# Performance work log

Measured on AMD Instinct MI355X. Metric: run time of the kernel, lower is better.

The kernel has to match this reference:

```python
import jax, jax.numpy as jnp
import numpy as np

B, T, D, H = 4, 2048, 1024, 16
DH = D // H

def setup_inputs() -> dict:
    key = jax.random.key(0)
    k1, k2, k3 = jax.random.split(key, 3)
    x = jax.random.normal(k1, (B, T, D), dtype=jnp.float32)
    w_qkv = jax.random.normal(k2, (D, 3 * D), dtype=jnp.float32) * (1.0 / np.sqrt(D))
    w_out = jax.random.normal(k3, (D, D), dtype=jnp.float32) * (1.0 / np.sqrt(D))
    return {"x": x, "w_qkv": w_qkv, "w_out": w_out}

def reference(x, w_qkv, w_out):
    Bq, Tq, C = x.shape
    qkv = x @ w_qkv                                   # [B,T,3D]
    q, k, v = jnp.split(qkv, 3, axis=-1)
    q = q.reshape(Bq, Tq, H, DH).transpose(0, 2, 1, 3)  # [B,H,T,dh]
    k = k.reshape(Bq, Tq, H, DH).transpose(0, 2, 1, 3)
    v = v.reshape(Bq, Tq, H, DH).transpose(0, 2, 1, 3)
    scores = jnp.einsum('bhqd,bhkd->bhqk', q, k) / jnp.sqrt(jnp.float32(DH))
    mask = jnp.tril(jnp.ones((Tq, Tq), dtype=bool))
    scores = jnp.where(mask, scores, jnp.float32(-jnp.inf))
    attn = jax.nn.softmax(scores, axis=-1)
    out = jnp.einsum('bhqk,bhkd->bhqd', attn, v)      # [B,H,T,dh]
    out = out.transpose(0, 2, 1, 3).reshape(Bq, Tq, C)
    return out @ w_out
```

## Files before the change

### kernel.cpp

```cpp
#include <hip/hip_runtime.h>

#define B_ 4
#define T_ 2048
#define D_ 1024
#define H_ 16
#define DH_ 64
#define BH_ (B_*H_)
#define M_ (B_*T_)
#define N3_ (3*D_)

typedef __attribute__((ext_vector_type(8))) __bf16 bf16x8;
typedef __attribute__((ext_vector_type(4))) float f32x4;
typedef __attribute__((ext_vector_type(16))) float f32x16;
typedef __attribute__((ext_vector_type(8))) unsigned short u16x8;
typedef __attribute__((ext_vector_type(4))) unsigned short u16x4;
typedef int i32x2 __attribute__((ext_vector_type(2)));

__device__ inline void gload_lds16(const void* g, void* l) {
  __builtin_amdgcn_global_load_lds((const __attribute__((address_space(1))) void*)g,
                                   (__attribute__((address_space(3))) void*)l, 16, 0, 0);
}

__device__ inline unsigned short f2bf(float v) {
  __bf16 t = (__bf16)v;
  return *(unsigned short*)&t;
}

__device__ inline unsigned pk2(float lo, float hi2) {
  return (unsigned)f2bf(lo) | ((unsigned)f2bf(hi2) << 16);
}

template<int BASE>
__device__ inline bf16x8 buildP(const f32x16& S) {
  unsigned a = pk2(S[BASE+0], S[BASE+1]);
  unsigned b = pk2(S[BASE+2], S[BASE+3]);
  unsigned c = pk2(S[BASE+4], S[BASE+5]);
  unsigned d = pk2(S[BASE+6], S[BASE+7]);
  i32x2 r0 = __builtin_amdgcn_permlane32_swap((int)a, (int)c, false, false);
  i32x2 r1 = __builtin_amdgcn_permlane32_swap((int)b, (int)d, false, false);
  union { unsigned u[4]; bf16x8 v; } U;
  U.u[0] = (unsigned)r0[0];
  U.u[1] = (unsigned)r1[0];
  U.u[2] = (unsigned)r0[1];
  U.u[3] = (unsigned)r1[1];
  return U.v;
}

__global__ void prep(const float* __restrict__ x, unsigned short* __restrict__ xb,
                     const float* __restrict__ wq, unsigned short* __restrict__ wqT,
                     const float* __restrict__ wo, unsigned short* __restrict__ woT) {
  __shared__ unsigned short lds[64][72];
  int bid = blockIdx.x, tid = threadIdx.x;
  if (bid < 4096) {
    int i = bid * 256 + tid;
    const float4* p = (const float4*)(x + (size_t)i * 8);
    float4 a = p[0], b = p[1];
    float v[8] = {a.x, a.y, a.z, a.w, b.x, b.y, b.z, b.w};
    u16x8 r;
#pragma unroll
    for (int j = 0; j < 8; ++j) r[j] = f2bf(v[j]);
    *(u16x8*)(xb + (size_t)i * 8) = r;
    return;
  }
  const float* w;
  unsigned short* wt;
  int n0, k0, Ndim;
  if (bid < 4096 + 768) {
    int b2 = bid - 4096;
    w = wq; wt = wqT; Ndim = N3_;
    n0 = (b2 % 48) * 64; k0 = (b2 / 48) * 64;
  } else {
    int b3 = bid - 4864;
    w = wo; wt = woT; Ndim = D_;
    n0 = (b3 % 16) * 64; k0 = (b3 / 16) * 64;
  }
#pragma unroll
  for (int i = 0; i < 2; ++i) {
    int idx = i * 256 + tid;
    int r = idx >> 3, c8 = idx & 7;
    const float4* src = (const float4*)(w + (size_t)(k0 + r) * Ndim + n0 + c8 * 8);
    float4 a = src[0], b = src[1];
    float v[8] = {a.x, a.y, a.z, a.w, b.x, b.y, b.z, b.w};
#pragma unroll
    for (int j = 0; j < 8; ++j) lds[r][c8 * 8 + j] = f2bf(v[j]);
  }
  __syncthreads();
#pragma unroll
  for (int i = 0; i < 2; ++i) {
    int idx = i * 256 + tid;
    int r = idx >> 3, c8 = idx & 7;
    u16x8 o;
#pragma unroll
    for (int j = 0; j < 8; ++j) o[j] = lds[c8 * 8 + j][r];
    *(u16x8*)(wt + (size_t)(n0 + r) * 1024 + k0 + c8 * 8) = o;
  }
}

__global__ __launch_bounds__(512) void gemm8p(
    const unsigned short* __restrict__ A,
    const unsigned short* __restrict__ BT,
    int epi,
    unsigned short* __restrict__ qb, unsigned short* __restrict__ kb, unsigned short* __restrict__ vtb,
    float* __restrict__ outf) {
  extern __shared__ __align__(16) char lds[];
  const int tid = threadIdx.x;
  const int wave = tid >> 6, lane = tid & 63, g = lane >> 4, c = lane & 15;
  const int wm = wave >> 2, wn = wave & 3;
  int flat = blockIdx.y * gridDim.x + blockIdx.x;
  int xcd = flat & 7, local = flat >> 3;
  int bx = xcd * 8 + (local & 7);
  int by = local >> 3;
  const int m0 = bx * 128, n0 = by * 256;

  f32x4 acc[4][4] = {};

  auto stage3 = [&](int slot, int jj, int half) {
    char* sb = lds + slot * 49152;
#pragma unroll
    for (int q = 0; q < 3; ++q) {
      int qq = half * 3 + q;
      if (qq < 2) {
        int idx = qq * 512 + tid;
        int r = idx >> 3, s = idx & 7;
        gload_lds16(A + (size_t)(m0 + r) * 1024 + jj * 64 + 8 * (s ^ (r & 7)),
                    sb + idx * 16);
      } else {
        int idx = (qq - 2) * 512 + tid;
        int r = idx >> 3, s = idx & 7;
        gload_lds16(BT + (size_t)(n0 + r) * 1024 + jj * 64 + 8 * (s ^ (r & 7)),
                    sb + 16384 + idx * 16);
      }
    }
  };

  stage3(0, 0, 0); stage3(0, 0, 1);
  stage3(1, 1, 0); stage3(1, 1, 1);

  int sj = 0;
  for (int j = 0; j < 16; ++j) {
    const int jj = (j + 2 < 16) ? j + 2 : 15;
    int st2 = sj + 2; if (st2 >= 3) st2 -= 3;
    const char* sA = lds + sj * 49152;
    const char* sB = sA + 16384;

    stage3(st2, jj, 0);
    asm volatile("s_waitcnt vmcnt(9)" ::: "memory");
    __builtin_amdgcn_s_barrier();
    asm volatile("" ::: "memory");

    {
      bf16x8 af[4], bf[4];
#pragma unroll
      for (int mt = 0; mt < 4; ++mt) {
        int r = wm * 64 + mt * 16 + c;
        af[mt] = *(const bf16x8*)(sA + r * 128 + 16 * (g ^ (r & 7)));
      }
#pragma unroll
      for (int nt = 0; nt < 4; ++nt) {
        int r = wn * 64 + nt * 16 + c;
        bf[nt] = *(const bf16x8*)(sB + r * 128 + 16 * (g ^ (r & 7)));
      }
      __builtin_amdgcn_s_setprio(1);
#pragma unroll
      for (int mt = 0; mt < 4; ++mt)
#pragma unroll
        for (int nt = 0; nt < 4; ++nt)
          acc[mt][nt] = __builtin_amdgcn_mfma_f32_16x16x32_bf16(af[mt], bf[nt], acc[mt][nt], 0, 0, 0);
      __builtin_amdgcn_s_setprio(0);
    }

    stage3(st2, jj, 1);

    {
      bf16x8 af[4], bf[4];
#pragma unroll
      for (int mt = 0; mt < 4; ++mt) {
        int r = wm * 64 + mt * 16 + c;
        af[mt] = *(const bf16x8*)(sA + r * 128 + 16 * ((4 + g) ^ (r & 7)));
      }
#pragma unroll
      for (int nt = 0; nt < 4; ++nt) {
        int r = wn * 64 + nt * 16 + c;
        bf[nt] = *(const bf16x8*)(sB + r * 128 + 16 * ((4 + g) ^ (r & 7)));
      }
      __builtin_amdgcn_s_setprio(1);
#pragma unroll
      for (int mt = 0; mt < 4; ++mt)
#pragma unroll
        for (int nt = 0; nt < 4; ++nt)
          acc[mt][nt] = __builtin_amdgcn_mfma_f32_16x16x32_bf16(af[mt], bf[nt], acc[mt][nt], 0, 0, 0);
      __builtin_amdgcn_s_setprio(0);
    }

    __builtin_amdgcn_s_barrier();
    asm volatile("" ::: "memory");
    sj = sj + 1; if (sj >= 3) sj -= 3;
  }

  if (epi == 0) {
    int which = n0 >> 10;
    int colbase = n0 - (which << 10);
    if (which == 2) {
#pragma unroll
      for (int mt = 0; mt < 4; ++mt)
#pragma unroll
        for (int nt = 0; nt < 4; ++nt) {
          int m = m0 + wm * 64 + mt * 16 + g * 4;
          int n = colbase + wn * 64 + nt * 16 + c;
          int b = m >> 11, t = m & 2047;
          int h = n >> 6, d = n & 63;
          u16x4 pk;
#pragma unroll
          for (int i = 0; i < 4; ++i) pk[i] = f2bf(acc[mt][nt][i]);
          *(u16x4*)(vtb + ((size_t)(b * H_ + h) * 64 + d) * T_ + t) = pk;
        }
    } else {
      unsigned short* dst = which == 0 ? qb : kb;
      float scale = which == 0 ? 0.18033688011112042f : 1.0f;
#pragma unroll
      for (int mt = 0; mt < 4; ++mt)
#pragma unroll
        for (int nt = 0; nt < 4; ++nt)
#pragma unroll
          for (int i = 0; i < 4; ++i) {
            int m = m0 + wm * 64 + mt * 16 + g * 4 + i;
            int n = colbase + wn * 64 + nt * 16 + c;
            int b = m >> 11, t = m & 2047;
            int h = n >> 6, d = n & 63;
            dst[(((size_t)(b * H_ + h) * T_ + t) << 6) + d] = f2bf(acc[mt][nt][i] * scale);
          }
    }
  } else {
#pragma unroll
    for (int mt = 0; mt < 4; ++mt)
#pragma unroll
      for (int nt = 0; nt < 4; ++nt)
#pragma unroll
        for (int i = 0; i < 4; ++i) {
          int m = m0 + wm * 64 + mt * 16 + g * 4 + i;
          int n = n0 + wn * 64 + nt * 16 + c;
          outf[(size_t)m * 1024 + n] = acc[mt][nt][i];
        }
  }
}

#define PV_STEP(PF, KC)                                                                \
  {                                                                                    \
    bf16x8 pf = (PF);                                                                  \
    int dr0 = q32, dr1 = 32 + q32;                                                     \
    bf16x8 v0 = *(const bf16x8*)(sV + dr0 * 128 + 16 * (((KC)*2 + hi) ^ (dr0 & 7)));   \
    bf16x8 v1 = *(const bf16x8*)(sV + dr1 * 128 + 16 * (((KC)*2 + hi) ^ (dr1 & 7)));   \
    oT0 = __builtin_amdgcn_mfma_f32_32x32x16_bf16(v0, pf, oT0, 0, 0, 0);               \
    oT1 = __builtin_amdgcn_mfma_f32_32x32x16_bf16(v1, pf, oT1, 0, 0, 0);               \
  }

__global__ __launch_bounds__(512) void attn(
    const unsigned short* __restrict__ qbp,
    const unsigned short* __restrict__ kb,
    const unsigned short* __restrict__ vt,
    unsigned short* __restrict__ ao) {
  __shared__ __align__(16) char pool[49152];
  const int tid = threadIdx.x;
  const int wave = tid >> 6, lane = tid & 63;
  const int q32 = lane & 31, hi = lane >> 5;
  const int bh = blockIdx.y;
  const int flip = (bh >> 5) & 1;
  const int pb = flip ? blockIdx.x : (T_ / 256 - 1) - blockIdx.x;
  const int q0w = pb * 256 + wave * 32;
  const int kmax = 4 * pb + 3;
  const int dtile = 4 * pb + (wave >> 1);

  bf16x8 qf[4];
#pragma unroll
  for (int dhc = 0; dhc < 4; ++dhc)
    qf[dhc] = *(const bf16x8*)(qbp + ((size_t)bh * T_ + q0w + q32) * 64 + dhc * 16 + hi * 8);

  f32x16 oT0 = {}, oT1 = {};
  float l_run = 0.0f;

  auto stage = [&](int buf, int kt) {
    int r = tid >> 3, s8 = tid & 7;
    gload_lds16(kb + ((size_t)bh * T_ + kt * 64 + r) * 64 + 8 * (s8 ^ (r & 7)),
                pool + buf * 16384 + tid * 16);
    gload_lds16(vt + ((size_t)bh * 64 + r) * T_ + kt * 64 + 8 * (s8 ^ (r & 7)),
                pool + buf * 16384 + 8192 + tid * 16);
  };

  stage(0, 0);
  stage(1, 1);
  int sj = 0;
  for (int kt = 0; kt <= kmax; ++kt) {
    asm volatile("s_waitcnt vmcnt(2)" ::: "memory");
    __builtin_amdgcn_s_barrier();
    asm volatile("" ::: "memory");
    int st2 = sj + 2; if (st2 >= 3) st2 -= 3;
    if (kt + 2 <= kmax) stage(st2, kt + 2);
    if (kt <= dtile) {
      const char* sK = pool + sj * 16384;
      const char* sV = sK + 8192;

      f32x16 st0 = {}, st1 = {};
      __builtin_amdgcn_s_setprio(1);
#pragma unroll
      for (int dhc = 0; dhc < 4; ++dhc) {
        int kr0 = q32, kr1 = 32 + q32;
        bf16x8 k0 = *(const bf16x8*)(sK + kr0 * 128 + 16 * ((dhc * 2 + hi) ^ (kr0 & 7)));
        bf16x8 k1 = *(const bf16x8*)(sK + kr1 * 128 + 16 * ((dhc * 2 + hi) ^ (kr1 & 7)));
        st0 = __builtin_amdgcn_mfma_f32_32x32x16_bf16(k0, qf[dhc], st0, 0, 0, 0);
        st1 = __builtin_amdgcn_mfma_f32_32x32x16_bf16(k1, qf[dhc], st1, 0, 0, 0);
      }
      __builtin_amdgcn_s_setprio(0);

      if (kt == dtile) {
        int qg = q0w + q32;
#pragma unroll
        for (int r = 0; r < 16; ++r) {
          int krow = kt * 64 + (r & 3) + 8 * (r >> 2) + 4 * hi;
          if (krow > qg) st0[r] = -INFINITY;
          if (krow + 32 > qg) st1[r] = -INFINITY;
        }
      }

      float ps0 = 0.0f, ps1 = 0.0f, ps2 = 0.0f, ps3 = 0.0f;
#pragma unroll
      for (int r = 0; r < 16; r += 4) {
        float a0 = __builtin_amdgcn_exp2f(st0[r + 0]); st0[r + 0] = a0; ps0 += a0;
        float a1 = __builtin_amdgcn_exp2f(st0[r + 1]); st0[r + 1] = a1; ps1 += a1;
        float a2 = __builtin_amdgcn_exp2f(st0[r + 2]); st0[r + 2] = a2; ps2 += a2;
        float a3 = __builtin_amdgcn_exp2f(st0[r + 3]); st0[r + 3] = a3; ps3 += a3;
      }
#pragma unroll
      for (int r = 0; r < 16; r += 4) {
        float a0 = __builtin_amdgcn_exp2f(st1[r + 0]); st1[r + 0] = a0; ps0 += a0;
        float a1 = __builtin_amdgcn_exp2f(st1[r + 1]); st1[r + 1] = a1; ps1 += a1;
        float a2 = __builtin_amdgcn_exp2f(st1[r + 2]); st1[r + 2] = a2; ps2 += a2;
        float a3 = __builtin_amdgcn_exp2f(st1[r + 3]); st1[r + 3] = a3; ps3 += a3;
      }
      float ps = (ps0 + ps1) + (ps2 + ps3);
      ps += __shfl_xor(ps, 32);
      l_run += ps;

      __builtin_amdgcn_s_setprio(1);
      PV_STEP(buildP<0>(st0), 0)
      PV_STEP(buildP<8>(st0), 1)
      PV_STEP(buildP<0>(st1), 2)
      PV_STEP(buildP<8>(st1), 3)
      __builtin_amdgcn_s_setprio(0);
    }
    sj = sj + 1; if (sj >= 3) sj -= 3;
  }

  __syncthreads();
  unsigned short* ep = (unsigned short*)pool + wave * (32 * 72);
  float inv_l = 1.0f / l_run;
#pragma unroll
  for (int r = 0; r < 16; ++r) {
    int d0 = (r & 3) + 8 * (r >> 2) + 4 * hi;
    ep[q32 * 72 + d0]      = f2bf(oT0[r] * inv_l);
    ep[q32 * 72 + 32 + d0] = f2bf(oT1[r] * inv_l);
  }
  __syncthreads();
  {
    int q = lane >> 1, half = lane & 1;
    int t = q0w + q;
    int b = bh >> 4, h = bh & 15;
    const unsigned short* row = ep + q * 72 + half * 32;
    unsigned short* g = ao + ((size_t)(b * T_ + t)) * 1024 + h * 64 + half * 32;
#pragma unroll
    for (int j = 0; j < 4; ++j)
      *(u16x8*)(g + j * 8) = *(const u16x8*)(row + j * 8);
  }
}

extern "C" void kernel_launch(void* const* d_in, const int* in_sizes, int n_in,
                              void* d_out, int out_size, void* d_ws, size_t ws_size,
                              hipStream_t stream) {
  const float* x = (const float*)d_in[0];
  const float* w_qkv = (const float*)d_in[1];
  const float* w_out = (const float*)d_in[2];
  float* out = (float*)d_out;

  char* ws = (char*)d_ws;
  size_t off = 0;
  auto alloc = [&](size_t bytes) {
    char* p = ws + off;
    off += (bytes + 255) & ~(size_t)255;
    return p;
  };
  unsigned short* xb    = (unsigned short*)alloc((size_t)M_ * D_ * 2);
  unsigned short* wqkvT = (unsigned short*)alloc((size_t)N3_ * D_ * 2);
  unsigned short* woutT = (unsigned short*)alloc((size_t)D_ * D_ * 2);
  unsigned short* qbuf  = (unsigned short*)alloc((size_t)BH_ * T_ * 64 * 2);
  unsigned short* kbuf  = (unsigned short*)alloc((size_t)BH_ * T_ * 64 * 2);
  unsigned short* vtb   = (unsigned short*)alloc((size_t)BH_ * 64 * T_ * 2);
  unsigned short* ao    = xb;

  hipFuncSetAttribute(reinterpret_cast<const void*>(gemm8p),
                      hipFuncAttributeMaxDynamicSharedMemorySize, 147456);

  prep<<<4096 + 768 + 256, 256, 0, stream>>>(x, xb, w_qkv, wqkvT, w_out, woutT);
  gemm8p<<<dim3(M_ / 128, N3_ / 256), 512, 147456, stream>>>(xb, wqkvT, 0, qbuf, kbuf, vtb, nullptr);
  attn<<<dim3(T_ / 256, BH_), 512, 0, stream>>>(qbuf, kbuf, vtb, ao);
  gemm8p<<<dim3(M_ / 128, D_ / 256), 512, 147456, stream>>>(ao, woutT, 1, nullptr, nullptr, nullptr, out);
}
```

Before: 152.6 us.

## Shrink GEMM tile to 128x128 with 4 waves and double-buffered LDS

Replaces the 128x256, 8-wave, triple-buffered GEMM with a 128x128, 4-wave kernel that double-buffers 64-wide K slices in 64KB of LDS. Each K step issues one full prefetch of the next slice and then runs both 32-wide K halves. The smaller LDS footprint and block size should let more blocks fit per CU and doubles the grid size, improving occupancy and load balance. The cost is less operand reuse per tile and a shallower prefetch pipeline, so global and LDS traffic per FLOP rises and load latency is less hidden.

```diff
diff --git a/kernel.cpp b/kernel.cpp
--- a/kernel.cpp
+++ b/kernel.cpp
@@ -96,7 +96,7 @@
   }
 }
 
-__global__ __launch_bounds__(512) void gemm8p(
+__global__ __launch_bounds__(256) void gemm2b(
     const unsigned short* __restrict__ A,
     const unsigned short* __restrict__ BT,
     int epi,
@@ -105,60 +105,58 @@
   extern __shared__ __align__(16) char lds[];
   const int tid = threadIdx.x;
   const int wave = tid >> 6, lane = tid & 63, g = lane >> 4, c = lane & 15;
-  const int wm = wave >> 2, wn = wave & 3;
+  const int wm = wave >> 1, wn = wave & 1;
   int flat = blockIdx.y * gridDim.x + blockIdx.x;
   int xcd = flat & 7, local = flat >> 3;
   int bx = xcd * 8 + (local & 7);
   int by = local >> 3;
-  const int m0 = bx * 128, n0 = by * 256;
+  const int m0 = bx * 128, n0 = by * 128;
 
   f32x4 acc[4][4] = {};
 
-  auto stage3 = [&](int slot, int jj, int half) {
-    char* sb = lds + slot * 49152;
-#pragma unroll
-    for (int q = 0; q < 3; ++q) {
-      int qq = half * 3 + q;
-      if (qq < 2) {
-        int idx = qq * 512 + tid;
-        int r = idx >> 3, s = idx & 7;
-        gload_lds16(A + (size_t)(m0 + r) * 1024 + jj * 64 + 8 * (s ^ (r & 7)),
-                    sb + idx * 16);
-      } else {
-        int idx = (qq - 2) * 512 + tid;
-        int r = idx >> 3, s = idx & 7;
-        gload_lds16(BT + (size_t)(n0 + r) * 1024 + jj * 64 + 8 * (s ^ (r & 7)),
-                    sb + 16384 + idx * 16);
-      }
+  auto stage = [&](int slot, int jj) {
+    char* sb = lds + slot * 32768;
+#pragma unroll
+    for (int i = 0; i < 4; ++i) {
+      int idx = i * 256 + tid;
+      int r = idx >> 3, s = idx & 7;
+      gload_lds16(A + (size_t)(m0 + r) * 1024 + jj * 64 + 8 * (s ^ (r & 7)),
+                  sb + idx * 16);
+    }
+#pragma unroll
+    for (int i = 0; i < 4; ++i) {
+      int idx = i * 256 + tid;
+      int r = idx >> 3, s = idx & 7;
+      gload_lds16(BT + (size_t)(n0 + r) * 1024 + jj * 64 + 8 * (s ^ (r & 7)),
+                  sb + 16384 + idx * 16);
     }
   };
 
-  stage3(0, 0, 0); stage3(0, 0, 1);
-  stage3(1, 1, 0); stage3(1, 1, 1);
-
-  int sj = 0;
+  stage(0, 0);
   for (int j = 0; j < 16; ++j) {
-    const int jj = (j + 2 < 16) ? j + 2 : 15;
-    int st2 = sj + 2; if (st2 >= 3) st2 -= 3;
-    const char* sA = lds + sj * 49152;
-    const char* sB = sA + 16384;
-
-    stage3(st2, jj, 0);
-    asm volatile("s_waitcnt vmcnt(9)" ::: "memory");
+    if (j < 15) {
+      stage((j + 1) & 1, j + 1);
+      asm volatile("s_waitcnt vmcnt(8)" ::: "memory");
+    } else {
+      asm volatile("s_waitcnt vmcnt(0)" ::: "memory");
+    }
     __builtin_amdgcn_s_barrier();
     asm volatile("" ::: "memory");
 
-    {
+    const char* sA = lds + (j & 1) * 32768;
+    const char* sB = sA + 16384;
+#pragma unroll
+    for (int kc = 0; kc < 2; ++kc) {
       bf16x8 af[4], bf[4];
 #pragma unroll
       for (int mt = 0; mt < 4; ++mt) {
         int r = wm * 64 + mt * 16 + c;
-        af[mt] = *(const bf16x8*)(sA + r * 128 + 16 * (g ^ (r & 7)));
+        af[mt] = *(const bf16x8*)(sA + r * 128 + 16 * ((kc * 4 + g) ^ (r & 7)));
       }
 #pragma unroll
       for (int nt = 0; nt < 4; ++nt) {
         int r = wn * 64 + nt * 16 + c;
-        bf[nt] = *(const bf16x8*)(sB + r * 128 + 16 * (g ^ (r & 7)));
+        bf[nt] = *(const bf16x8*)(sB + r * 128 + 16 * ((kc * 4 + g) ^ (r & 7)));
       }
       __builtin_amdgcn_s_setprio(1);
 #pragma unroll
@@ -169,32 +167,8 @@
       __builtin_amdgcn_s_setprio(0);
     }
 
-    stage3(st2, jj, 1);
-
-    {
-      bf16x8 af[4], bf[4];
-#pragma unroll
-      for (int mt = 0; mt < 4; ++mt) {
-        int r = wm * 64 + mt * 16 + c;
-        af[mt] = *(const bf16x8*)(sA + r * 128 + 16 * ((4 + g) ^ (r & 7)));
-      }
-#pragma unroll
-      for (int nt = 0; nt < 4; ++nt) {
-        int r = wn * 64 + nt * 16 + c;
-        bf[nt] = *(const bf16x8*)(sB + r * 128 + 16 * ((4 + g) ^ (r & 7)));
-      }
-      __builtin_amdgcn_s_setprio(1);
-#pragma unroll
-      for (int mt = 0; mt < 4; ++mt)
-#pragma unroll
-        for (int nt = 0; nt < 4; ++nt)
-          acc[mt][nt] = __builtin_amdgcn_mfma_f32_16x16x32_bf16(af[mt], bf[nt], acc[mt][nt], 0, 0, 0);
-      __builtin_amdgcn_s_setprio(0);
-    }
-
     __builtin_amdgcn_s_barrier();
     asm volatile("" ::: "memory");
-    sj = sj + 1; if (sj >= 3) sj -= 3;
   }
 
   if (epi == 0) {
@@ -395,11 +369,11 @@
   unsigned short* vtb   = (unsigned short*)alloc((size_t)BH_ * 64 * T_ * 2);
   unsigned short* ao    = xb;
 
-  hipFuncSetAttribute(reinterpret_cast<const void*>(gemm8p),
-                      hipFuncAttributeMaxDynamicSharedMemorySize, 147456);
+  hipFuncSetAttribute(reinterpret_cast<const void*>(gemm2b),
+                      hipFuncAttributeMaxDynamicSharedMemorySize, 65536);
 
   prep<<<4096 + 768 + 256, 256, 0, stream>>>(x, xb, w_qkv, wqkvT, w_out, woutT);
-  gemm8p<<<dim3(M_ / 128, N3_ / 256), 512, 147456, stream>>>(xb, wqkvT, 0, qbuf, kbuf, vtb, nullptr);
+  gemm2b<<<dim3(M_ / 128, N3_ / 128), 256, 65536, stream>>>(xb, wqkvT, 0, qbuf, kbuf, vtb, nullptr);
   attn<<<dim3(T_ / 256, BH_), 512, 0, stream>>>(qbuf, kbuf, vtb, ao);
-  gemm8p<<<dim3(M_ / 128, D_ / 256), 512, 147456, stream>>>(ao, woutT, 1, nullptr, nullptr, nullptr, out);
-}
+  gemm2b<<<dim3(M_ / 128, D_ / 128), 256, 65536, stream>>>(ao, woutT, 1, nullptr, nullptr, nullptr, out);
+}
```

New measurement: 148.9 us, median of 3. 1.03x faster.
